# Optimization experiments

Hardware: AMD Instinct MI355X
Metric: run time of the kernel (lower is better)

## Reference

```python
import jax, jax.numpy as jnp
import numpy as np

B, C, H, W = 32, 256, 64, 64
WS, SHIFT, HEADS = 8, 4, 8
DK, L = C // HEADS, WS * WS
NW = (H // WS) * (W // WS)


def _rel_index():
    coords = np.stack(np.meshgrid(np.arange(WS), np.arange(WS), indexing='ij')).reshape(2, -1)
    rel = (coords[:, :, None] - coords[:, None, :]).transpose(1, 2, 0)
    rel[..., 0] += WS - 1
    rel[..., 1] += WS - 1
    rel[..., 0] *= 2 * WS - 1
    return rel.sum(-1)  # (L, L) int


def _attn_mask():
    img = np.zeros((H, W))
    sl = [slice(0, -WS), slice(-WS, -SHIFT), slice(-SHIFT, None)]
    cnt = 0
    for hs in sl:
        for ws_ in sl:
            img[hs, ws_] = cnt
            cnt += 1
    mw = img.reshape(H // WS, WS, W // WS, WS).transpose(0, 2, 1, 3).reshape(-1, L)
    diff = mw[:, None, :] - mw[:, :, None]
    return np.where(diff != 0, -100.0, 0.0).astype(np.float32)  # (NW, L, L)


REL_IDX = _rel_index()
MASK = jnp.asarray(_attn_mask())


def _conv1x1(w, b, t):
    return jnp.einsum('oc,bchw->bohw', w, t) + b[None, :, None, None]


def _shift(t, s):
    # 'double window': first half of channels unshifted, second half cyclically shifted
    a, b2 = jnp.split(t, 2, axis=1)
    return jnp.concatenate([a, jnp.roll(b2, (s, s), axis=(2, 3))], axis=1)


def _win_part(t):
    b = t.shape[0]
    t = t.reshape(b, C, H // WS, WS, W // WS, WS).transpose(0, 2, 4, 1, 3, 5)
    return t.reshape(-1, HEADS, DK, L)  # (B*NW, heads, d_k, L)


def _win_rev(t):
    t = t.reshape(-1, H // WS, W // WS, C, WS, WS).transpose(0, 3, 1, 4, 2, 5)
    return t.reshape(-1, C, H, W)


def setup_inputs() -> dict:
    key = jax.random.key(0)
    ks = jax.random.split(key, 6)
    return {
        'x': jax.random.normal(ks[0], (B, C, H, W), jnp.float32),
        'wq': jax.random.normal(ks[1], (C, C), jnp.float32) * 0.02,
        'bq': jnp.zeros((C,), jnp.float32),
        'wkv': jax.random.normal(ks[2], (2 * C, C), jnp.float32) * 0.02,
        'bkv': jnp.zeros((2 * C,), jnp.float32),
        'wproj': jax.random.normal(ks[3], (C, C), jnp.float32) * 0.02,
        'bproj': jnp.zeros((C,), jnp.float32),
        'rpb': jax.random.normal(ks[4], ((2 * WS - 1) ** 2, HEADS), jnp.float32) * 0.02,
    }


def reference(x, wq, bq, wkv, bkv, wproj, bproj, rpb):
    q = _conv1x1(wq, bq, x)
    k, v = jnp.split(_conv1x1(wkv, bkv, x), 2, axis=1)
    q, k, v = _shift(q, -SHIFT), _shift(k, -SHIFT), _shift(v, -SHIFT)
    q, k, v = _win_part(q), _win_part(k), _win_part(v)
    attn = jnp.einsum('bhct,bhcs->bhts', q, k) * (DK ** -0.5)
    bias = rpb[REL_IDX.reshape(-1)].reshape(L, L, HEADS).transpose(2, 0, 1)
    attn = attn + bias[None]
    attn = attn.reshape(-1, NW, HEADS, L, L) + MASK[None, :, None]
    attn = jax.nn.softmax(attn.reshape(-1, HEADS, L, L), axis=-1)
    out = jnp.einsum('bhts,bhcs->bhct', attn, v)
    out = _win_rev(out)
    out = _shift(out, SHIFT)
    return _conv1x1(wproj, bproj, out)
```

## Files before the change

kernel.cpp:

```cpp
#include <hip/hip_runtime.h>


typedef __attribute__((ext_vector_type(8))) short bf16x8;
typedef __attribute__((ext_vector_type(4))) float f32x4;

__device__ __forceinline__ ushort f2bf(float f) {
  uint u = __float_as_uint(f);
  return (ushort)((u + 0x7fffu + ((u >> 16) & 1u)) >> 16);
}

__global__ __launch_bounds__(256) void x2b_kernel(const float* __restrict__ in,
                                                  ushort* __restrict__ out) {
  const size_t i = ((size_t)blockIdx.x * 256 + threadIdx.x) * 4;
  const float4 f = *reinterpret_cast<const float4*>(in + i);
  ushort4 u;
  u.x = f2bf(f.x); u.y = f2bf(f.y); u.z = f2bf(f.z); u.w = f2bf(f.w);
  *reinterpret_cast<ushort4*>(out + i) = u;
}

__global__ __launch_bounds__(256) void w2b_kernel(const float* __restrict__ wq,
                                                  const float* __restrict__ wkv,
                                                  const float* __restrict__ wproj,
                                                  ushort* __restrict__ Wb) {
  const int i = (blockIdx.x * 256 + threadIdx.x) * 4;
  const int row = i >> 8;
  const float* src = (row < 256) ? (wq + i)
                   : (row < 768) ? (wkv + (i - 65536))
                                 : (wproj + (i - 196608));
  const float4 f = *reinterpret_cast<const float4*>(src);
  ushort4 u;
  u.x = f2bf(f.x); u.y = f2bf(f.y); u.z = f2bf(f.z); u.w = f2bf(f.w);
  *reinterpret_cast<ushort4*>(Wb + i) = u;
}

__global__ __launch_bounds__(256) void qkv_mfma_kernel(
    const ushort* __restrict__ xb, const ushort* __restrict__ Wb,
    const float* __restrict__ bq, const float* __restrict__ bkv,
    ushort* __restrict__ Qb, ushort* __restrict__ Kb, ushort* __restrict__ Vb) {
  const int ot = blockIdx.x;
  const int pt = blockIdx.y & 31;
  const int lb = blockIdx.y >> 5;
  const int pix0 = pt * 128;

  __shared__ __align__(16) ushort lds[2][2][8192];

  const int tid = threadIdx.x;
  const int l = tid & 63, wv = tid >> 6;
  const int wr = wv >> 1, wc = wv & 1;
  const int pg = tid & 31, cg = tid >> 5;
  const int kg = tid & 7, ocr = tid >> 3;
  const int l15 = l & 15, l4 = l >> 4;

  const ushort* Wsrc = Wb + (size_t)(ot * 128) * 256;
  const ushort* Xsrc = xb + ((size_t)lb << 20) + pix0;

  ushort4 xr[8];
  bf16x8 wreg[4];
  f32x4 acc[4][4] = {};

#define LOAD_REGS(KK)                                                         \
  {                                                                           \
    const int c0 = (KK) * 64;                                                 \
    _Pragma("unroll") for (int i = 0; i < 8; i++)                             \
        xr[i] = *reinterpret_cast<const ushort4*>(                            \
            Xsrc + ((size_t)(c0 + cg * 8 + i) << 12) + pg * 4);               \
    _Pragma("unroll") for (int ii = 0; ii < 4; ii++)                          \
        wreg[ii] = *reinterpret_cast<const bf16x8*>(                          \
            Wsrc + (size_t)(ocr + 32 * ii) * 256 + c0 + kg * 8);              \
  }

#define WRITE_LDS(BUF)                                                        \
  {                                                                           \
    ushort* Wt = &lds[(BUF)][0][0];                                           \
    ushort* Xt = &lds[(BUF)][1][0];                                           \
    _Pragma("unroll") for (int ii = 0; ii < 4; ii++) {                        \
      const int row = ocr + 32 * ii;                                          \
      *reinterpret_cast<bf16x8*>((char*)Wt + row * 128 +                      \
                                 ((kg * 16) ^ ((row & 7) << 4))) = wreg[ii];  \
    }                                                                         \
    _Pragma("unroll") for (int j = 0; j < 4; j++) {                           \
      const int row = pg * 4 + j;                                             \
      bf16x8 v;                                                               \
      _Pragma("unroll") for (int i = 0; i < 8; i++) {                         \
        const ushort e = (j == 0) ? xr[i].x                                   \
                       : (j == 1) ? xr[i].y                                   \
                       : (j == 2) ? xr[i].z : xr[i].w;                        \
        v[i] = (short)e;                                                      \
      }                                                                       \
      *reinterpret_cast<bf16x8*>((char*)Xt + row * 128 +                      \
                                 ((cg * 16) ^ ((row & 7) << 4))) = v;         \
    }                                                                         \
  }

  LOAD_REGS(0)
  WRITE_LDS(0)
  __syncthreads();

#pragma unroll
  for (int kk = 0; kk < 4; kk++) {
    if (kk < 3) LOAD_REGS(kk + 1)
    const ushort* Wt = &lds[kk & 1][0][0];
    const ushort* Xt = &lds[kk & 1][1][0];
#pragma unroll
    for (int ks = 0; ks < 2; ks++) {
      bf16x8 a[4], b[4];
      const int colB = ks * 64 + (l4 << 4);
#pragma unroll
      for (int m = 0; m < 4; m++) {
        const int row = wr * 64 + m * 16 + l15;
        a[m] = *reinterpret_cast<const bf16x8*>(
            (const char*)Wt + row * 128 + (colB ^ ((row & 7) << 4)));
      }
#pragma unroll
      for (int n = 0; n < 4; n++) {
        const int row = wc * 64 + n * 16 + l15;
        b[n] = *reinterpret_cast<const bf16x8*>(
            (const char*)Xt + row * 128 + (colB ^ ((row & 7) << 4)));
      }
#pragma unroll
      for (int m = 0; m < 4; m++)
#pragma unroll
        for (int n = 0; n < 4; n++)
          acc[m][n] = __builtin_amdgcn_mfma_f32_16x16x32_bf16(a[m], b[n],
                                                              acc[m][n], 0, 0, 0);
    }
    if (kk < 3) {
      WRITE_LDS((kk + 1) & 1)
      __syncthreads();
    }
  }

  const float scale = 0.17677669529663687f;
  const int mode = ot >> 1;
#pragma unroll
  for (int m = 0; m < 4; m++) {
    const int ob = ot * 128 + wr * 64 + m * 16 + (l4 << 2);
    const int ch = ob & 255;
    const int head = (ch >> 5) & 7;
    const int c0 = ch & 31;
    const bool sh = (ch & 128) != 0;
    float bias[4];
#pragma unroll
    for (int r = 0; r < 4; r++)
      bias[r] = (mode == 0) ? bq[ob + r] : bkv[ob + r - 256];
#pragma unroll
    for (int n = 0; n < 4; n++) {
      const int P = pix0 + wc * 64 + n * 16 + l15;
      const int h = P >> 6, w = P & 63;
      int hh = h, ww2 = w;
      if (sh) { hh = (h + 60) & 63; ww2 = (w + 60) & 63; }
      const int wi = ((hh >> 3) << 3) + (ww2 >> 3);
      const int l2 = ((hh & 7) << 3) + (ww2 & 7);
      const size_t base = ((size_t)(lb * 64 + wi) * 8 + head) << 11;
      if (mode == 2) {
#pragma unroll
        for (int r = 0; r < 4; r++)
          Vb[base + (size_t)(c0 + r) * 64 + l2] = f2bf(acc[m][n][r] + bias[r]);
      } else {
        ushort4 pk;
        float v0 = acc[m][n][0] + bias[0], v1 = acc[m][n][1] + bias[1];
        float v2 = acc[m][n][2] + bias[2], v3 = acc[m][n][3] + bias[3];
        if (mode == 0) { v0 *= scale; v1 *= scale; v2 *= scale; v3 *= scale; }
        pk.x = f2bf(v0); pk.y = f2bf(v1); pk.z = f2bf(v2); pk.w = f2bf(v3);
        ushort* qk = (mode == 0) ? Qb : Kb;
        *reinterpret_cast<ushort4*>(qk + base + (l2 << 5) + c0) = pk;
      }
    }
  }
#undef LOAD_REGS
#undef WRITE_LDS
}

__global__ __launch_bounds__(256) void attn_kernel(
    const ushort* __restrict__ Qb, const ushort* __restrict__ Kb,
    const ushort* __restrict__ Vb, const float* __restrict__ rpb,
    ushort* __restrict__ Y) {
  const int bwh = blockIdx.x;
  const int head = bwh & 7;
  const int bw = bwh >> 3;
  const int wi = bw & 63;
  const int lb = bw >> 6;
  const int wh = wi >> 3, ww = wi & 7;

  __shared__ __align__(16) ushort Qs[2048];
  __shared__ __align__(16) ushort Ks[2048];
  __shared__ __align__(16) ushort Vs[2048];
  __shared__ __align__(16) ushort Ps[4096];
  __shared__ float Rs[232];

  const int tid = threadIdx.x;
  const size_t gbase = (size_t)bwh << 11;

  {
    const int lq = tid >> 2, cq = tid & 3;
    const uint4 qv = *reinterpret_cast<const uint4*>(Qb + gbase + lq * 32 + cq * 8);
    const uint4 kv = *reinterpret_cast<const uint4*>(Kb + gbase + lq * 32 + cq * 8);
    *reinterpret_cast<uint4*>((char*)Qs + lq * 64 + ((cq * 16) ^ ((lq & 3) << 4))) = qv;
    *reinterpret_cast<uint4*>((char*)Ks + lq * 64 + ((cq * 16) ^ ((lq & 3) << 4))) = kv;
    const int cv = tid >> 3, s8 = tid & 7;
    const uint4 vv = *reinterpret_cast<const uint4*>(Vb + gbase + cv * 64 + s8 * 8);
    *reinterpret_cast<uint4*>((char*)Vs + cv * 128 + ((s8 * 16) ^ ((cv & 7) << 4))) = vv;
    if (tid < 225) Rs[tid] = rpb[tid * 8 + head];
  }
  __syncthreads();

  const int l = tid & 63, wv = tid >> 6;
  const int t0 = wv * 16;
  const int l15 = l & 15, l4 = l >> 4;

  f32x4 accQ[4] = {};
  {
    const int tr = t0 + l15;
    const bf16x8 af = *reinterpret_cast<const bf16x8*>(
        (const char*)Qs + tr * 64 + ((l4 * 16) ^ ((tr & 3) << 4)));
#pragma unroll
    for (int nt = 0; nt < 4; nt++) {
      const int s = nt * 16 + l15;
      const bf16x8 bfv = *reinterpret_cast<const bf16x8*>(
          (const char*)Ks + s * 64 + ((l4 * 16) ^ ((s & 3) << 4)));
      accQ[nt] = __builtin_amdgcn_mfma_f32_16x16x32_bf16(af, bfv, accQ[nt], 0, 0, 0);
    }
  }

#pragma unroll
  for (int nt = 0; nt < 4; nt++) {
    const int s = nt * 16 + l15;
    const int si = s >> 3, sj = s & 7;
    const int hs = wh * 8 + si, wsx = ww * 8 + sj;
    const int cls = (hs < 56 ? 0 : (hs < 60 ? 1 : 2)) * 3 +
                    (wsx < 56 ? 0 : (wsx < 60 ? 1 : 2));
#pragma unroll
    for (int r = 0; r < 4; r++) {
      const int t = t0 + l4 * 4 + r;
      const int ri = t >> 3, rj = t & 7;
      const int hr = wh * 8 + ri, wrx = ww * 8 + rj;
      const int clr = (hr < 56 ? 0 : (hr < 60 ? 1 : 2)) * 3 +
                      (wrx < 56 ? 0 : (wrx < 60 ? 1 : 2));
      float add = Rs[(ri - si + 7) * 15 + (rj - sj + 7)];
      if (clr != cls) add -= 100.f;
      accQ[nt][r] += add;
    }
  }

#pragma unroll
  for (int r = 0; r < 4; r++) {
    float mx = fmaxf(fmaxf(accQ[0][r], accQ[1][r]), fmaxf(accQ[2][r], accQ[3][r]));
#pragma unroll
    for (int off = 1; off < 16; off <<= 1) mx = fmaxf(mx, __shfl_xor(mx, off));
    float e0 = __expf(accQ[0][r] - mx), e1 = __expf(accQ[1][r] - mx);
    float e2 = __expf(accQ[2][r] - mx), e3 = __expf(accQ[3][r] - mx);
    float sm = (e0 + e1) + (e2 + e3);
#pragma unroll
    for (int off = 1; off < 16; off <<= 1) sm += __shfl_xor(sm, off);
    const float rinv = 1.0f / sm;
    const int t = t0 + l4 * 4 + r;
    const int swz = (t & 7) << 4;
    *(ushort*)((char*)Ps + t * 128 + (((0 * 16 + l15) * 2) ^ swz)) = f2bf(e0 * rinv);
    *(ushort*)((char*)Ps + t * 128 + (((1 * 16 + l15) * 2) ^ swz)) = f2bf(e1 * rinv);
    *(ushort*)((char*)Ps + t * 128 + (((2 * 16 + l15) * 2) ^ swz)) = f2bf(e2 * rinv);
    *(ushort*)((char*)Ps + t * 128 + (((3 * 16 + l15) * 2) ^ swz)) = f2bf(e3 * rinv);
  }

  f32x4 acc2[2] = {};
#pragma unroll
  for (int kk = 0; kk < 2; kk++) {
    const int colb = kk * 64 + l4 * 16;
    const int tr = t0 + l15;
    const bf16x8 b2 = *reinterpret_cast<const bf16x8*>(
        (const char*)Ps + tr * 128 + (colb ^ ((tr & 7) << 4)));
#pragma unroll
    for (int mt = 0; mt < 2; mt++) {
      const int c = mt * 16 + l15;
      const bf16x8 a2 = *reinterpret_cast<const bf16x8*>(
          (const char*)Vs + c * 128 + (colb ^ ((c & 7) << 4)));
      acc2[mt] = __builtin_amdgcn_mfma_f32_16x16x32_bf16(a2, b2, acc2[mt], 0, 0, 0);
    }
  }

  __syncthreads();

#pragma unroll
  for (int mt = 0; mt < 2; mt++)
#pragma unroll
    for (int r = 0; r < 4; r++) {
      const int c = mt * 16 + l4 * 4 + r;
      const int t = t0 + l15;
      *(ushort*)((char*)Qs + c * 128 + ((t * 2) ^ ((c & 7) << 4))) =
          f2bf(acc2[mt][r]);
    }
  __syncthreads();

  {
    const int c = tid >> 3, chunk = tid & 7;
    const uint4 v = *reinterpret_cast<const uint4*>(
        (const char*)Qs + c * 128 + ((chunk * 16) ^ ((c & 7) << 4)));
    const int ch = head * 32 + c;
    const int hh = wh * 8 + chunk;
    *reinterpret_cast<uint4*>(Y + (((size_t)lb * 256 + ch) << 12) + hh * 64 +
                              ww * 8) = v;
  }
}

__global__ __launch_bounds__(256) void proj_mfma_kernel(
    const ushort* __restrict__ Yb, const ushort* __restrict__ Wb,
    const float* __restrict__ bproj, float* __restrict__ out, int b0) {
  const int ot = blockIdx.x;
  const int pt = blockIdx.y & 31;
  const int lb = blockIdx.y >> 5;
  const int pix0 = pt * 128;

  __shared__ __align__(16) ushort lds[2][2][8192];

  const int tid = threadIdx.x;
  const int l = tid & 63, wv = tid >> 6;
  const int wr = wv >> 1, wc = wv & 1;
  const int pg = tid & 31, cg = tid >> 5;
  const int kg = tid & 7, ocr = tid >> 3;
  const int l15 = l & 15, l4 = l >> 4;

  const ushort* Wsrc = Wb + (size_t)(768 + ot * 128) * 256;
  const ushort* Ysrc = Yb + ((size_t)lb << 20);

  const int P0 = pix0 + pg * 4;
  const int h0 = P0 >> 6, w0 = P0 & 63;
  const int Psh = ((h0 + 60) & 63) * 64 + ((w0 + 60) & 63);

  ushort4 xr[8];
  bf16x8 wreg[4];
  f32x4 acc[4][4] = {};

#define LOAD_REGS_C(KK)                                                       \
  {                                                                           \
    const int c0 = (KK) * 64;                                                 \
    const int srcP = (c0 & 128) ? Psh : P0;                                   \
    _Pragma("unroll") for (int i = 0; i < 8; i++)                             \
        xr[i] = *reinterpret_cast<const ushort4*>(                            \
            Ysrc + ((size_t)(c0 + cg * 8 + i) << 12) + srcP);                 \
    _Pragma("unroll") for (int ii = 0; ii < 4; ii++)                          \
        wreg[ii] = *reinterpret_cast<const bf16x8*>(                          \
            Wsrc + (size_t)(ocr + 32 * ii) * 256 + c0 + kg * 8);              \
  }

#define WRITE_LDS_C(BUF)                                                      \
  {                                                                           \
    ushort* Wt = &lds[(BUF)][0][0];                                           \
    ushort* Xt = &lds[(BUF)][1][0];                                           \
    _Pragma("unroll") for (int ii = 0; ii < 4; ii++) {                        \
      const int row = ocr + 32 * ii;                                          \
      *reinterpret_cast<bf16x8*>((char*)Wt + row * 128 +                      \
                                 ((kg * 16) ^ ((row & 7) << 4))) = wreg[ii];  \
    }                                                                         \
    _Pragma("unroll") for (int j = 0; j < 4; j++) {                           \
      const int row = pg * 4 + j;                                             \
      bf16x8 v;                                                               \
      _Pragma("unroll") for (int i = 0; i < 8; i++) {                         \
        const ushort e = (j == 0) ? xr[i].x                                   \
                       : (j == 1) ? xr[i].y                                   \
                       : (j == 2) ? xr[i].z : xr[i].w;                        \
        v[i] = (short)e;                                                      \
      }                                                                       \
      *reinterpret_cast<bf16x8*>((char*)Xt + row * 128 +                      \
                                 ((cg * 16) ^ ((row & 7) << 4))) = v;         \
    }                                                                         \
  }

  LOAD_REGS_C(0)
  WRITE_LDS_C(0)
  __syncthreads();

#pragma unroll
  for (int kk = 0; kk < 4; kk++) {
    if (kk < 3) LOAD_REGS_C(kk + 1)
    const ushort* Wt = &lds[kk & 1][0][0];
    const ushort* Xt = &lds[kk & 1][1][0];
#pragma unroll
    for (int ks = 0; ks < 2; ks++) {
      bf16x8 a[4], b[4];
      const int colB = ks * 64 + (l4 << 4);
#pragma unroll
      for (int m = 0; m < 4; m++) {
        const int row = wr * 64 + m * 16 + l15;
        a[m] = *reinterpret_cast<const bf16x8*>(
            (const char*)Wt + row * 128 + (colB ^ ((row & 7) << 4)));
      }
#pragma unroll
      for (int n = 0; n < 4; n++) {
        const int row = wc * 64 + n * 16 + l15;
        b[n] = *reinterpret_cast<const bf16x8*>(
            (const char*)Xt + row * 128 + (colB ^ ((row & 7) << 4)));
      }
#pragma unroll
      for (int m = 0; m < 4; m++)
#pragma unroll
        for (int n = 0; n < 4; n++)
          acc[m][n] = __builtin_amdgcn_mfma_f32_16x16x32_bf16(a[m], b[n],
                                                              acc[m][n], 0, 0, 0);
    }
    if (kk < 3) {
      WRITE_LDS_C((kk + 1) & 1)
      __syncthreads();
    }
  }

  const int b = b0 + lb;
#pragma unroll
  for (int m = 0; m < 4; m++) {
#pragma unroll
    for (int r = 0; r < 4; r++) {
      const int o = ot * 128 + wr * 64 + m * 16 + (l4 << 2) + r;
      const float bias = bproj[o];
#pragma unroll
      for (int n = 0; n < 4; n++) {
        const int P = pix0 + wc * 64 + n * 16 + l15;
        out[(((size_t)b * 256 + o) << 12) + P] = acc[m][n][r] + bias;
      }
    }
  }
#undef LOAD_REGS_C
#undef WRITE_LDS_C
}

extern "C" void kernel_launch(void* const* d_in, const int* in_sizes, int n_in,
                              void* d_out, int out_size, void* d_ws,
                              size_t ws_size, hipStream_t stream) {
  const float* x = (const float*)d_in[0];
  const float* wq = (const float*)d_in[1];
  const float* bq = (const float*)d_in[2];
  const float* wkv = (const float*)d_in[3];
  const float* bkv = (const float*)d_in[4];
  const float* wproj = (const float*)d_in[5];
  const float* bproj = (const float*)d_in[6];
  const float* rpb = (const float*)d_in[7];
  float* out = (float*)d_out;

  const size_t perB = 1048576ull;
  const size_t wbBytes = 1024ull * 256ull * 2ull;
  const size_t perBatchBytes = 5ull * perB * 2ull;

  int chunk = (int)((ws_size > wbBytes ? ws_size - wbBytes : 0) / perBatchBytes);
  if (chunk > 32) chunk = 32;
  if (chunk < 1) chunk = 1;

  char* p = (char*)d_ws;
  ushort* Wb = (ushort*)p; p += wbBytes;
  ushort* xb = (ushort*)p; p += (size_t)chunk * perB * 2;
  ushort* Qb = (ushort*)p; p += (size_t)chunk * perB * 2;
  ushort* Kb = (ushort*)p; p += (size_t)chunk * perB * 2;
  ushort* Vb = (ushort*)p; p += (size_t)chunk * perB * 2;
  ushort* Yb = (ushort*)p;

  w2b_kernel<<<256, 256, 0, stream>>>(wq, wkv, wproj, Wb);

  for (int b0 = 0; b0 < 32; b0 += chunk) {
    const int cb = (32 - b0 < chunk) ? (32 - b0) : chunk;
    x2b_kernel<<<cb * 1024, 256, 0, stream>>>(x + (size_t)b0 * perB, xb);
    qkv_mfma_kernel<<<dim3(6, cb * 32), 256, 0, stream>>>(xb, Wb, bq, bkv,
                                                          Qb, Kb, Vb);
    attn_kernel<<<cb * 512, 256, 0, stream>>>(Qb, Kb, Vb, rpb, Yb);
    proj_mfma_kernel<<<dim3(2, cb * 32), 256, 0, stream>>>(Yb, Wb, bproj,
                                                           out, b0);
  }
}
```

Baseline: 478.6 us.

## Fuse x→bf16 conversion into QKV GEMM and move shift/window gather into attention

Drops the separate x2b conversion kernel: the QKV GEMM now reads fp32 x directly and converts it to bf16 while staging into LDS. The K tile is halved to 32 with twice as many iterations and a new swizzle. Q/K are stored pixel-major and V channel-major with no window permutation, and the attention kernel applies the cyclic shift and window gather on load. This removes one full read/write pass over x and a workspace buffer. In exchange the GEMM reads twice the global bytes for x, and the attention loads become scattered (split uint2 loads for shifted V).

```diff
diff --git a/kernel.cpp b/kernel.cpp
--- a/kernel.cpp
+++ b/kernel.cpp
@@ -9,14 +9,7 @@
   return (ushort)((u + 0x7fffu + ((u >> 16) & 1u)) >> 16);
 }
 
-__global__ __launch_bounds__(256) void x2b_kernel(const float* __restrict__ in,
-                                                  ushort* __restrict__ out) {
-  const size_t i = ((size_t)blockIdx.x * 256 + threadIdx.x) * 4;
-  const float4 f = *reinterpret_cast<const float4*>(in + i);
-  ushort4 u;
-  u.x = f2bf(f.x); u.y = f2bf(f.y); u.z = f2bf(f.z); u.w = f2bf(f.w);
-  *reinterpret_cast<ushort4*>(out + i) = u;
-}
+#define SWZ2(r) ((((r) & 3) ^ (((r) >> 2) & 3)) << 4)
 
 __global__ __launch_bounds__(256) void w2b_kernel(const float* __restrict__ wq,
                                                   const float* __restrict__ wkv,
@@ -34,61 +27,63 @@
 }
 
 __global__ __launch_bounds__(256) void qkv_mfma_kernel(
-    const ushort* __restrict__ xb, const ushort* __restrict__ Wb,
+    const float* __restrict__ x, const ushort* __restrict__ Wb,
     const float* __restrict__ bq, const float* __restrict__ bkv,
-    ushort* __restrict__ Qb, ushort* __restrict__ Kb, ushort* __restrict__ Vb) {
+    ushort* __restrict__ Qp, ushort* __restrict__ Kp, ushort* __restrict__ Vc,
+    int b0) {
   const int ot = blockIdx.x;
   const int pt = blockIdx.y & 31;
   const int lb = blockIdx.y >> 5;
   const int pix0 = pt * 128;
 
-  __shared__ __align__(16) ushort lds[2][2][8192];
+  __shared__ __align__(16) ushort lds[2][2][4096];
 
   const int tid = threadIdx.x;
   const int l = tid & 63, wv = tid >> 6;
   const int wr = wv >> 1, wc = wv & 1;
-  const int pg = tid & 31, cg = tid >> 5;
-  const int kg = tid & 7, ocr = tid >> 3;
   const int l15 = l & 15, l4 = l >> 4;
+  const int w_oc = tid >> 1, w_part = tid & 1;
+  const int pg = tid & 31, cq = tid >> 5;
 
   const ushort* Wsrc = Wb + (size_t)(ot * 128) * 256;
-  const ushort* Xsrc = xb + ((size_t)lb << 20) + pix0;
-
-  ushort4 xr[8];
-  bf16x8 wreg[4];
+  const float* Xsrc = x + ((size_t)(b0 + lb) << 20) + pix0;
+
+  float4 xr[4];
+  bf16x8 wreg[2];
   f32x4 acc[4][4] = {};
 
 #define LOAD_REGS(KK)                                                         \
   {                                                                           \
-    const int c0 = (KK) * 64;                                                 \
-    _Pragma("unroll") for (int i = 0; i < 8; i++)                             \
-        xr[i] = *reinterpret_cast<const ushort4*>(                            \
-            Xsrc + ((size_t)(c0 + cg * 8 + i) << 12) + pg * 4);               \
-    _Pragma("unroll") for (int ii = 0; ii < 4; ii++)                          \
-        wreg[ii] = *reinterpret_cast<const bf16x8*>(                          \
-            Wsrc + (size_t)(ocr + 32 * ii) * 256 + c0 + kg * 8);              \
+    const int c0 = (KK) * 32;                                                 \
+    _Pragma("unroll") for (int i = 0; i < 4; i++)                             \
+        xr[i] = *reinterpret_cast<const float4*>(                             \
+            Xsrc + ((size_t)(c0 + cq * 4 + i) << 12) + pg * 4);               \
+    _Pragma("unroll") for (int k = 0; k < 2; k++)                             \
+        wreg[k] = *reinterpret_cast<const bf16x8*>(                           \
+            Wsrc + (size_t)w_oc * 256 + c0 + w_part * 16 + k * 8);            \
   }
 
 #define WRITE_LDS(BUF)                                                        \
   {                                                                           \
     ushort* Wt = &lds[(BUF)][0][0];                                           \
     ushort* Xt = &lds[(BUF)][1][0];                                           \
-    _Pragma("unroll") for (int ii = 0; ii < 4; ii++) {                        \
-      const int row = ocr + 32 * ii;                                          \
-      *reinterpret_cast<bf16x8*>((char*)Wt + row * 128 +                      \
-                                 ((kg * 16) ^ ((row & 7) << 4))) = wreg[ii];  \
-    }                                                                         \
+    _Pragma("unroll") for (int k = 0; k < 2; k++)                             \
+        *reinterpret_cast<bf16x8*>(                                           \
+            (char*)Wt + w_oc * 64 +                                           \
+            ((w_part * 32 + k * 16) ^ SWZ2(w_oc))) = wreg[k];                 \
     _Pragma("unroll") for (int j = 0; j < 4; j++) {                           \
       const int row = pg * 4 + j;                                             \
-      bf16x8 v;                                                               \
-      _Pragma("unroll") for (int i = 0; i < 8; i++) {                         \
-        const ushort e = (j == 0) ? xr[i].x                                   \
-                       : (j == 1) ? xr[i].y                                   \
-                       : (j == 2) ? xr[i].z : xr[i].w;                        \
-        v[i] = (short)e;                                                      \
-      }                                                                       \
-      *reinterpret_cast<bf16x8*>((char*)Xt + row * 128 +                      \
-                                 ((cg * 16) ^ ((row & 7) << 4))) = v;         \
+      ushort4 v;                                                              \
+      v.x = f2bf(j == 0 ? xr[0].x : j == 1 ? xr[0].y : j == 2 ? xr[0].z       \
+                                                              : xr[0].w);     \
+      v.y = f2bf(j == 0 ? xr[1].x : j == 1 ? xr[1].y : j == 2 ? xr[1].z       \
+                                                              : xr[1].w);     \
+      v.z = f2bf(j == 0 ? xr[2].x : j == 1 ? xr[2].y : j == 2 ? xr[2].z       \
+                                                              : xr[2].w);     \
+      v.w = f2bf(j == 0 ? xr[3].x : j == 1 ? xr[3].y : j == 2 ? xr[3].z       \
+                                                              : xr[3].w);     \
+      *reinterpret_cast<ushort4*>((char*)Xt + row * 64 +                      \
+                                  ((cq * 8) ^ SWZ2(row))) = v;                \
     }                                                                         \
   }
 
@@ -97,73 +92,64 @@
   __syncthreads();
 
 #pragma unroll
-  for (int kk = 0; kk < 4; kk++) {
-    if (kk < 3) LOAD_REGS(kk + 1)
+  for (int kk = 0; kk < 8; kk++) {
+    if (kk < 7) LOAD_REGS(kk + 1)
     const ushort* Wt = &lds[kk & 1][0][0];
     const ushort* Xt = &lds[kk & 1][1][0];
-#pragma unroll
-    for (int ks = 0; ks < 2; ks++) {
-      bf16x8 a[4], b[4];
-      const int colB = ks * 64 + (l4 << 4);
-#pragma unroll
-      for (int m = 0; m < 4; m++) {
-        const int row = wr * 64 + m * 16 + l15;
-        a[m] = *reinterpret_cast<const bf16x8*>(
-            (const char*)Wt + row * 128 + (colB ^ ((row & 7) << 4)));
-      }
-#pragma unroll
-      for (int n = 0; n < 4; n++) {
-        const int row = wc * 64 + n * 16 + l15;
-        b[n] = *reinterpret_cast<const bf16x8*>(
-            (const char*)Xt + row * 128 + (colB ^ ((row & 7) << 4)));
-      }
-#pragma unroll
-      for (int m = 0; m < 4; m++)
-#pragma unroll
-        for (int n = 0; n < 4; n++)
-          acc[m][n] = __builtin_amdgcn_mfma_f32_16x16x32_bf16(a[m], b[n],
-                                                              acc[m][n], 0, 0, 0);
-    }
-    if (kk < 3) {
+    bf16x8 a[4], bfr[4];
+#pragma unroll
+    for (int m = 0; m < 4; m++) {
+      const int row = wr * 64 + m * 16 + l15;
+      a[m] = *reinterpret_cast<const bf16x8*>(
+          (const char*)Wt + row * 64 + ((l4 * 16) ^ SWZ2(row)));
+    }
+#pragma unroll
+    for (int n = 0; n < 4; n++) {
+      const int row = wc * 64 + n * 16 + l15;
+      bfr[n] = *reinterpret_cast<const bf16x8*>(
+          (const char*)Xt + row * 64 + ((l4 * 16) ^ SWZ2(row)));
+    }
+#pragma unroll
+    for (int m = 0; m < 4; m++)
+#pragma unroll
+      for (int n = 0; n < 4; n++)
+        acc[m][n] = __builtin_amdgcn_mfma_f32_16x16x32_bf16(a[m], bfr[n],
+                                                            acc[m][n], 0, 0, 0);
+    if (kk < 7) {
       WRITE_LDS((kk + 1) & 1)
       __syncthreads();
     }
   }
 
-  const float scale = 0.17677669529663687f;
   const int mode = ot >> 1;
+  const float scale = (mode == 0) ? 0.17677669529663687f : 1.0f;
 #pragma unroll
   for (int m = 0; m < 4; m++) {
-    const int ob = ot * 128 + wr * 64 + m * 16 + (l4 << 2);
-    const int ch = ob & 255;
-    const int head = (ch >> 5) & 7;
-    const int c0 = ch & 31;
-    const bool sh = (ch & 128) != 0;
-    float bias[4];
-#pragma unroll
-    for (int r = 0; r < 4; r++)
-      bias[r] = (mode == 0) ? bq[ob + r] : bkv[ob + r - 256];
-#pragma unroll
-    for (int n = 0; n < 4; n++) {
-      const int P = pix0 + wc * 64 + n * 16 + l15;
-      const int h = P >> 6, w = P & 63;
-      int hh = h, ww2 = w;
-      if (sh) { hh = (h + 60) & 63; ww2 = (w + 60) & 63; }
-      const int wi = ((hh >> 3) << 3) + (ww2 >> 3);
-      const int l2 = ((hh & 7) << 3) + (ww2 & 7);
-      const size_t base = ((size_t)(lb * 64 + wi) * 8 + head) << 11;
-      if (mode == 2) {
-#pragma unroll
-        for (int r = 0; r < 4; r++)
-          Vb[base + (size_t)(c0 + r) * 64 + l2] = f2bf(acc[m][n][r] + bias[r]);
-      } else {
-        ushort4 pk;
-        float v0 = acc[m][n][0] + bias[0], v1 = acc[m][n][1] + bias[1];
-        float v2 = acc[m][n][2] + bias[2], v3 = acc[m][n][3] + bias[3];
-        if (mode == 0) { v0 *= scale; v1 *= scale; v2 *= scale; v3 *= scale; }
-        pk.x = f2bf(v0); pk.y = f2bf(v1); pk.z = f2bf(v2); pk.w = f2bf(v3);
-        ushort* qk = (mode == 0) ? Qb : Kb;
-        *reinterpret_cast<ushort4*>(qk + base + (l2 << 5) + c0) = pk;
+    const int o0 = ot * 128 + wr * 64 + m * 16 + (l4 << 2);
+    const int ch0 = o0 & 255;
+    const float4 b4 = *reinterpret_cast<const float4*>(
+        (mode == 0) ? (bq + o0) : (bkv + o0 - 256));
+    if (mode < 2) {
+      ushort* dst = (mode == 0) ? Qp : Kp;
+#pragma unroll
+      for (int n = 0; n < 4; n++) {
+        const int px = pix0 + wc * 64 + n * 16 + l15;
+        ushort4 st;
+        st.x = f2bf((acc[m][n][0] + b4.x) * scale);
+        st.y = f2bf((acc[m][n][1] + b4.y) * scale);
+        st.z = f2bf((acc[m][n][2] + b4.z) * scale);
+        st.w = f2bf((acc[m][n][3] + b4.w) * scale);
+        *reinterpret_cast<ushort4*>(
+            dst + (((size_t)lb << 12) + px) * 256 + ch0) = st;
+      }
+    } else {
+#pragma unroll
+      for (int n = 0; n < 4; n++) {
+        const int px = pix0 + wc * 64 + n * 16 + l15;
+        Vc[((size_t)(lb * 256 + ch0 + 0) << 12) + px] = f2bf(acc[m][n][0] + b4.x);
+        Vc[((size_t)(lb * 256 + ch0 + 1) << 12) + px] = f2bf(acc[m][n][1] + b4.y);
+        Vc[((size_t)(lb * 256 + ch0 + 2) << 12) + px] = f2bf(acc[m][n][2] + b4.z);
+        Vc[((size_t)(lb * 256 + ch0 + 3) << 12) + px] = f2bf(acc[m][n][3] + b4.w);
       }
     }
   }
@@ -172,8 +158,8 @@
 }
 
 __global__ __launch_bounds__(256) void attn_kernel(
-    const ushort* __restrict__ Qb, const ushort* __restrict__ Kb,
-    const ushort* __restrict__ Vb, const float* __restrict__ rpb,
+    const ushort* __restrict__ Qp, const ushort* __restrict__ Kp,
+    const ushort* __restrict__ Vc, const float* __restrict__ rpb,
     ushort* __restrict__ Y) {
   const int bwh = blockIdx.x;
   const int head = bwh & 7;
@@ -189,17 +175,34 @@
   __shared__ float Rs[232];
 
   const int tid = threadIdx.x;
-  const size_t gbase = (size_t)bwh << 11;
+  const ushort* Qsrc = Qp + ((size_t)lb << 20);
+  const ushort* Ksrc = Kp + ((size_t)lb << 20);
+  const ushort* Vsrc = Vc + ((size_t)lb << 20);
 
   {
-    const int lq = tid >> 2, cq = tid & 3;
-    const uint4 qv = *reinterpret_cast<const uint4*>(Qb + gbase + lq * 32 + cq * 8);
-    const uint4 kv = *reinterpret_cast<const uint4*>(Kb + gbase + lq * 32 + cq * 8);
-    *reinterpret_cast<uint4*>((char*)Qs + lq * 64 + ((cq * 16) ^ ((lq & 3) << 4))) = qv;
-    *reinterpret_cast<uint4*>((char*)Ks + lq * 64 + ((cq * 16) ^ ((lq & 3) << 4))) = kv;
-    const int cv = tid >> 3, s8 = tid & 7;
-    const uint4 vv = *reinterpret_cast<const uint4*>(Vb + gbase + cv * 64 + s8 * 8);
-    *reinterpret_cast<uint4*>((char*)Vs + cv * 128 + ((s8 * 16) ^ ((cv & 7) << 4))) = vv;
+    const int lq = tid >> 2, part = tid & 3;
+    const int i = lq >> 3, j = lq & 7;
+    int hh, wcol;
+    if (head < 4) { hh = wh * 8 + i; wcol = ww * 8 + j; }
+    else { hh = (wh * 8 + i + 4) & 63; wcol = (ww * 8 + j + 4) & 63; }
+    const size_t poff = ((size_t)(hh * 64 + wcol)) * 256 + head * 32 + part * 8;
+    const uint4 qv = *reinterpret_cast<const uint4*>(Qsrc + poff);
+    const uint4 kv = *reinterpret_cast<const uint4*>(Ksrc + poff);
+    *reinterpret_cast<uint4*>((char*)Qs + lq * 64 + ((part * 16) ^ SWZ2(lq))) = qv;
+    *reinterpret_cast<uint4*>((char*)Ks + lq * 64 + ((part * 16) ^ SWZ2(lq))) = kv;
+    const int cv = tid >> 3, iv = tid & 7;
+    const ushort* vrow;
+    uint4 vv;
+    if (head < 4) {
+      vrow = Vsrc + ((size_t)(head * 32 + cv) << 12) + (wh * 8 + iv) * 64;
+      vv = *reinterpret_cast<const uint4*>(vrow + ww * 8);
+    } else {
+      vrow = Vsrc + ((size_t)(head * 32 + cv) << 12) + (((wh * 8 + iv + 4) & 63) * 64);
+      const uint2 lo = *reinterpret_cast<const uint2*>(vrow + (ww * 8 + 4));
+      const uint2 hi = *reinterpret_cast<const uint2*>(vrow + ((ww * 8 + 8) & 63));
+      vv = make_uint4(lo.x, lo.y, hi.x, hi.y);
+    }
+    *reinterpret_cast<uint4*>((char*)Vs + cv * 128 + ((iv * 16) ^ ((cv & 7) << 4))) = vv;
     if (tid < 225) Rs[tid] = rpb[tid * 8 + head];
   }
   __syncthreads();
@@ -212,12 +215,12 @@
   {
     const int tr = t0 + l15;
     const bf16x8 af = *reinterpret_cast<const bf16x8*>(
-        (const char*)Qs + tr * 64 + ((l4 * 16) ^ ((tr & 3) << 4)));
+        (const char*)Qs + tr * 64 + ((l4 * 16) ^ SWZ2(tr)));
 #pragma unroll
     for (int nt = 0; nt < 4; nt++) {
       const int s = nt * 16 + l15;
       const bf16x8 bfv = *reinterpret_cast<const bf16x8*>(
-          (const char*)Ks + s * 64 + ((l4 * 16) ^ ((s & 3) << 4)));
+          (const char*)Ks + s * 64 + ((l4 * 16) ^ SWZ2(s)));
       accQ[nt] = __builtin_amdgcn_mfma_f32_16x16x32_bf16(af, bfv, accQ[nt], 0, 0, 0);
     }
   }
@@ -309,14 +312,14 @@
   const int lb = blockIdx.y >> 5;
   const int pix0 = pt * 128;
 
-  __shared__ __align__(16) ushort lds[2][2][8192];
+  __shared__ __align__(16) ushort lds[2][2][4096];
 
   const int tid = threadIdx.x;
   const int l = tid & 63, wv = tid >> 6;
   const int wr = wv >> 1, wc = wv & 1;
-  const int pg = tid & 31, cg = tid >> 5;
-  const int kg = tid & 7, ocr = tid >> 3;
   const int l15 = l & 15, l4 = l >> 4;
+  const int w_oc = tid >> 1, w_part = tid & 1;
+  const int pg = tid & 31, cq = tid >> 5;
 
   const ushort* Wsrc = Wb + (size_t)(768 + ot * 128) * 256;
   const ushort* Ysrc = Yb + ((size_t)lb << 20);
@@ -325,42 +328,43 @@
   const int h0 = P0 >> 6, w0 = P0 & 63;
   const int Psh = ((h0 + 60) & 63) * 64 + ((w0 + 60) & 63);
 
-  ushort4 xr[8];
-  bf16x8 wreg[4];
+  ushort4 xr[4];
+  bf16x8 wreg[2];
   f32x4 acc[4][4] = {};
 
 #define LOAD_REGS_C(KK)                                                       \
   {                                                                           \
-    const int c0 = (KK) * 64;                                                 \
+    const int c0 = (KK) * 32;                                                 \
     const int srcP = (c0 & 128) ? Psh : P0;                                   \
-    _Pragma("unroll") for (int i = 0; i < 8; i++)                             \
+    _Pragma("unroll") for (int i = 0; i < 4; i++)                             \
         xr[i] = *reinterpret_cast<const ushort4*>(                            \
-            Ysrc + ((size_t)(c0 + cg * 8 + i) << 12) + srcP);                 \
-    _Pragma("unroll") for (int ii = 0; ii < 4; ii++)                          \
-        wreg[ii] = *reinterpret_cast<const bf16x8*>(                          \
-            Wsrc + (size_t)(ocr + 32 * ii) * 256 + c0 + kg * 8);              \
+            Ysrc + ((size_t)(c0 + cq * 4 + i) << 12) + srcP);                 \
+    _Pragma("unroll") for (int k = 0; k < 2; k++)                             \
+        wreg[k] = *reinterpret_cast<const bf16x8*>(                           \
+            Wsrc + (size_t)w_oc * 256 + c0 + w_part * 16 + k * 8);            \
   }
 
 #define WRITE_LDS_C(BUF)                                                      \
   {                                                                           \
     ushort* Wt = &lds[(BUF)][0][0];                                           \
     ushort* Xt = &lds[(BUF)][1][0];                                           \
-    _Pragma("unroll") for (int ii = 0; ii < 4; ii++) {                        \
-      const int row = ocr + 32 * ii;                                          \
-      *reinterpret_cast<bf16x8*>((char*)Wt + row * 128 +                      \
-                                 ((kg * 16) ^ ((row & 7) << 4))) = wreg[ii];  \
-    }                                                                         \
+    _Pragma("unroll") for (int k = 0; k < 2; k++)                             \
+        *reinterpret_cast<bf16x8*>(                                           \
+            (char*)Wt + w_oc * 64 +                                           \
+            ((w_part * 32 + k * 16) ^ SWZ2(w_oc))) = wreg[k];                 \
     _Pragma("unroll") for (int j = 0; j < 4; j++) {                           \
       const int row = pg * 4 + j;                                             \
-      bf16x8 v;                                                               \
-      _Pragma("unroll") for (int i = 0; i < 8; i++) {                         \
-        const ushort e = (j == 0) ? xr[i].x                                   \
-                       : (j == 1) ? xr[i].y                                   \
-                       : (j == 2) ? xr[i].z : xr[i].w;                        \
-        v[i] = (short)e;                                                      \
-      }                                                                       \
-      *reinterpret_cast<bf16x8*>((char*)Xt + row * 128 +                      \
-                                 ((cg * 16) ^ ((row & 7) << 4))) = v;         \
+      ushort4 v;                                                              \
+      v.x = (j == 0) ? xr[0].x : (j == 1) ? xr[0].y : (j == 2) ? xr[0].z      \
+                                                               : xr[0].w;     \
+      v.y = (j == 0) ? xr[1].x : (j == 1) ? xr[1].y : (j == 2) ? xr[1].z      \
+                                                               : xr[1].w;     \
+      v.z = (j == 0) ? xr[2].x : (j == 1) ? xr[2].y : (j == 2) ? xr[2].z      \
+                                                               : xr[2].w;     \
+      v.w = (j == 0) ? xr[3].x : (j == 1) ? xr[3].y : (j == 2) ? xr[3].z      \
+                                                               : xr[3].w;     \
+      *reinterpret_cast<ushort4*>((char*)Xt + row * 64 +                      \
+                                  ((cq * 8) ^ SWZ2(row))) = v;                \
     }                                                                         \
   }
 
@@ -369,34 +373,30 @@
   __syncthreads();
 
 #pragma unroll
-  for (int kk = 0; kk < 4; kk++) {
-    if (kk < 3) LOAD_REGS_C(kk + 1)
+  for (int kk = 0; kk < 8; kk++) {
+    if (kk < 7) LOAD_REGS_C(kk + 1)
     const ushort* Wt = &lds[kk & 1][0][0];
     const ushort* Xt = &lds[kk & 1][1][0];
-#pragma unroll
-    for (int ks = 0; ks < 2; ks++) {
-      bf16x8 a[4], b[4];
-      const int colB = ks * 64 + (l4 << 4);
-#pragma unroll
-      for (int m = 0; m < 4; m++) {
-        const int row = wr * 64 + m * 16 + l15;
-        a[m] = *reinterpret_cast<const bf16x8*>(
-            (const char*)Wt + row * 128 + (colB ^ ((row & 7) << 4)));
-      }
-#pragma unroll
-      for (int n = 0; n < 4; n++) {
-        const int row = wc * 64 + n * 16 + l15;
-        b[n] = *reinterpret_cast<const bf16x8*>(
-            (const char*)Xt + row * 128 + (colB ^ ((row & 7) << 4)));
-      }
-#pragma unroll
-      for (int m = 0; m < 4; m++)
-#pragma unroll
-        for (int n = 0; n < 4; n++)
-          acc[m][n] = __builtin_amdgcn_mfma_f32_16x16x32_bf16(a[m], b[n],
-                                                              acc[m][n], 0, 0, 0);
-    }
-    if (kk < 3) {
+    bf16x8 a[4], bfr[4];
+#pragma unroll
+    for (int m = 0; m < 4; m++) {
+      const int row = wr * 64 + m * 16 + l15;
+      a[m] = *reinterpret_cast<const bf16x8*>(
+          (const char*)Wt + row * 64 + ((l4 * 16) ^ SWZ2(row)));
+    }
+#pragma unroll
+    for (int n = 0; n < 4; n++) {
+      const int row = wc * 64 + n * 16 + l15;
+      bfr[n] = *reinterpret_cast<const bf16x8*>(
+          (const char*)Xt + row * 64 + ((l4 * 16) ^ SWZ2(row)));
+    }
+#pragma unroll
+    for (int m = 0; m < 4; m++)
+#pragma unroll
+      for (int n = 0; n < 4; n++)
+        acc[m][n] = __builtin_amdgcn_mfma_f32_16x16x32_bf16(a[m], bfr[n],
+                                                            acc[m][n], 0, 0, 0);
+    if (kk < 7) {
       WRITE_LDS_C((kk + 1) & 1)
       __syncthreads();
     }
@@ -405,15 +405,15 @@
   const int b = b0 + lb;
 #pragma unroll
   for (int m = 0; m < 4; m++) {
-#pragma unroll
-    for (int r = 0; r < 4; r++) {
-      const int o = ot * 128 + wr * 64 + m * 16 + (l4 << 2) + r;
-      const float bias = bproj[o];
-#pragma unroll
-      for (int n = 0; n < 4; n++) {
-        const int P = pix0 + wc * 64 + n * 16 + l15;
-        out[(((size_t)b * 256 + o) << 12) + P] = acc[m][n][r] + bias;
-      }
+    const int o0 = ot * 128 + wr * 64 + m * 16 + (l4 << 2);
+    const float4 b4 = *reinterpret_cast<const float4*>(bproj + o0);
+#pragma unroll
+    for (int n = 0; n < 4; n++) {
+      const int P = pix0 + wc * 64 + n * 16 + l15;
+      out[(((size_t)b * 256 + o0 + 0) << 12) + P] = acc[m][n][0] + b4.x;
+      out[(((size_t)b * 256 + o0 + 1) << 12) + P] = acc[m][n][1] + b4.y;
+      out[(((size_t)b * 256 + o0 + 2) << 12) + P] = acc[m][n][2] + b4.z;
+      out[(((size_t)b * 256 + o0 + 3) << 12) + P] = acc[m][n][3] + b4.w;
     }
   }
 #undef LOAD_REGS_C
@@ -435,7 +435,7 @@
 
   const size_t perB = 1048576ull;
   const size_t wbBytes = 1024ull * 256ull * 2ull;
-  const size_t perBatchBytes = 5ull * perB * 2ull;
+  const size_t perBatchBytes = 4ull * perB * 2ull;
 
   int chunk = (int)((ws_size > wbBytes ? ws_size - wbBytes : 0) / perBatchBytes);
   if (chunk > 32) chunk = 32;
@@ -443,20 +443,18 @@
 
   char* p = (char*)d_ws;
   ushort* Wb = (ushort*)p; p += wbBytes;
-  ushort* xb = (ushort*)p; p += (size_t)chunk * perB * 2;
-  ushort* Qb = (ushort*)p; p += (size_t)chunk * perB * 2;
-  ushort* Kb = (ushort*)p; p += (size_t)chunk * perB * 2;
-  ushort* Vb = (ushort*)p; p += (size_t)chunk * perB * 2;
+  ushort* Qp = (ushort*)p; p += (size_t)chunk * perB * 2;
+  ushort* Kp = (ushort*)p; p += (size_t)chunk * perB * 2;
+  ushort* Vc = (ushort*)p; p += (size_t)chunk * perB * 2;
   ushort* Yb = (ushort*)p;
 
   w2b_kernel<<<256, 256, 0, stream>>>(wq, wkv, wproj, Wb);
 
   for (int b0 = 0; b0 < 32; b0 += chunk) {
     const int cb = (32 - b0 < chunk) ? (32 - b0) : chunk;
-    x2b_kernel<<<cb * 1024, 256, 0, stream>>>(x + (size_t)b0 * perB, xb);
-    qkv_mfma_kernel<<<dim3(6, cb * 32), 256, 0, stream>>>(xb, Wb, bq, bkv,
-                                                          Qb, Kb, Vb);
-    attn_kernel<<<cb * 512, 256, 0, stream>>>(Qb, Kb, Vb, rpb, Yb);
+    qkv_mfma_kernel<<<dim3(6, cb * 32), 256, 0, stream>>>(x, Wb, bq, bkv,
+                                                          Qp, Kp, Vc, b0);
+    attn_kernel<<<cb * 512, 256, 0, stream>>>(Qp, Kp, Vc, rpb, Yb);
     proj_mfma_kernel<<<dim3(2, cb * 32), 256, 0, stream>>>(Yb, Wb, bproj,
                                                            out, b0);
   }
```

Measured after the change: 503.7 us. +5.2%, slower.
